# Performance work log

Measured on AMD Instinct MI355X. Metric: run time of the kernel, lower is better.

Reference implementation:

```python
import jax, jax.numpy as jnp
import numpy as np

N_HEADS = 16
NEG_BIG = float(-2**32 + 1)  # value the original writes into masked positions


def setup_inputs() -> dict:
    key = jax.random.key(0)
    ks = jax.random.split(key, 5)
    B, T, D = 64, 256, 1024
    s = 1.0 / np.sqrt(D)
    return {
        "x": jax.random.normal(ks[0], (B, T, D), jnp.float32),
        "pos_emb": jax.random.normal(ks[1], (T, D), jnp.float32),
        "Wq": jax.random.normal(ks[2], (D, D), jnp.float32) * s,
        "Wk": jax.random.normal(ks[3], (D, D), jnp.float32) * s,
        "Wv": jax.random.normal(ks[4], (D, D), jnp.float32) * s,
    }


def reference(x, pos_emb, Wq, Wk, Wv):
    B, T, D = x.shape
    H = N_HEADS
    dh = D // H
    # add position embeddings (same arange positions for every batch row)
    temporal = x + pos_emb[None, :T, :]            # [B, T, D]
    q = temporal @ Wq                              # [B, T, D]
    k = temporal @ Wk
    v = temporal @ Wv
    # chunk along feature dim into H heads, concatenate along batch dim -> [H*B, T, dh]
    def split_heads(t):
        return jnp.concatenate(jnp.split(t, H, axis=2), axis=0)
    q_, k_, v_ = split_heads(q), split_heads(k), split_heads(v)
    scores = jnp.einsum('btd,bsd->bts', q_, k_) / jnp.sqrt(jnp.asarray(T, x.dtype))  # [H*B, T, T]
    # original masks the LOWER triangle (tril > 0 -> padding), faithful to source
    tril = jnp.tril(jnp.ones((T, T), x.dtype))
    scores = jnp.where(tril > 0, jnp.asarray(NEG_BIG, x.dtype), scores)
    # original applies softmax over dim=0 (the batch*head axis), faithful to source
    probs = jax.nn.softmax(scores, axis=0)         # [H*B, T, T]
    out = jnp.einsum('bts,bsd->btd', probs, v_)    # [H*B, T, dh]
    # merge heads back: chunk along batch dim, concatenate along feature dim
    out = jnp.concatenate(jnp.split(out, H, axis=0), axis=-1)  # [B, T, D]
    return out
```

## Files before the change

kernel.cpp:

```cpp
#include <hip/hip_runtime.h>

constexpr int SEQ = 256;
constexpr int DIM = 1024;
constexpr float SCALE = 0.0625f;

typedef __attribute__((ext_vector_type(8))) short bf16x8;
typedef __attribute__((ext_vector_type(4))) float f32x4;
typedef unsigned short ushort_t;
typedef unsigned int uint_t;

__device__ __forceinline__ void gld_lds16(const void* g, void* l) {
  __builtin_amdgcn_global_load_lds(
      (const __attribute__((address_space(1))) unsigned int*)g,
      (__attribute__((address_space(3))) unsigned int*)l, 16, 0, 0);
}

__device__ __forceinline__ ushort_t f2bf(float f) {
  uint_t u = __float_as_uint(f);
  return (ushort_t)((u + 0x7fffu + ((u >> 16) & 1u)) >> 16);
}

__global__ __launch_bounds__(256)
void prep_a(const float* __restrict__ x, const float* __restrict__ pos,
            ushort_t* __restrict__ Ab) {
  const size_t idx = ((size_t)blockIdx.x * 256 + threadIdx.x) * 8;
  const int m = (int)(idx >> 10), k = (int)(idx & 1023);
  float4 x0 = *(const float4*)(x + idx);
  float4 x1 = *(const float4*)(x + idx + 4);
  const float* pp = pos + ((size_t)(m & 255) << 10) + k;
  float4 p0 = *(const float4*)pp;
  float4 p1 = *(const float4*)(pp + 4);
  uint_t w0 = (uint_t)f2bf(x0.x + p0.x) | ((uint_t)f2bf(x0.y + p0.y) << 16);
  uint_t w1 = (uint_t)f2bf(x0.z + p0.z) | ((uint_t)f2bf(x0.w + p0.w) << 16);
  uint_t w2 = (uint_t)f2bf(x1.x + p1.x) | ((uint_t)f2bf(x1.y + p1.y) << 16);
  uint_t w3 = (uint_t)f2bf(x1.z + p1.z) | ((uint_t)f2bf(x1.w + p1.w) << 16);
  *(uint4*)&Ab[idx] = make_uint4(w0, w1, w2, w3);
}

__global__ __launch_bounds__(256)
void pack_w(const float* __restrict__ Wq, const float* __restrict__ Wk,
            const float* __restrict__ Wv, ushort_t* __restrict__ Bp) {
  const float* W = (blockIdx.z == 0) ? Wq : (blockIdx.z == 1) ? Wk : Wv;
  const int n  = blockIdx.x * 256 + threadIdx.x;
  const int k8 = blockIdx.y * 8;
  uint_t h[8];
#pragma unroll
  for (int i = 0; i < 8; ++i) h[i] = f2bf(W[(size_t)(k8 + i) * DIM + n]);
  uint_t hp[4];
#pragma unroll
  for (int j = 0; j < 4; ++j) hp[j] = h[2 * j] | (h[2 * j + 1] << 16);
  const int np = blockIdx.z * 1024 + n;
  const int nb = np >> 8, nl = np & 255;
  const int kc = k8 >> 6, kk = k8 & 63;
  size_t base = (((size_t)nb * 16 + kc) * 256 + nl) * 64 + kk;
  *(uint4*)&Bp[base] = make_uint4(hp[0], hp[1], hp[2], hp[3]);
}

__global__ __launch_bounds__(512, 2)
void qkv_mfma(const ushort_t* __restrict__ Ab, const ushort_t* __restrict__ Bp,
              ushort_t* __restrict__ q_bf, ushort_t* __restrict__ k_bf,
              ushort_t* __restrict__ vT_bf) {
  const int id = (int)blockIdx.x;
  const int q8 = id >> 3;
  const int nb = q8 % 12;
  const int mb = (id & 7) * 8 + q8 / 12;
  const int tid = (int)threadIdx.x;
  const int wave = tid >> 6, lane = tid & 63;
  const int wm = wave >> 2, wn = wave & 3;
  const int l15 = lane & 15, quad = lane >> 4;

  __shared__ ushort_t smem[65536];

  const int r8 = lane >> 3;
  const int lc8 = ((lane & 7) ^ r8) * 8;
  const size_t a_row = ((size_t)(mb * 256 + wave * 8 + r8)) << 10;
  const size_t b_row = ((size_t)((nb * 16) * 256 + wave * 8 + r8)) << 6;
  const int wb = wave * 512;

#define SA(q, tt, c) gld_lds16(Ab + a_row + ((size_t)(q) << 16) + (size_t)(tt) * 64 + lc8, \
                               smem + (c) * 32768 + (q) * 4096 + wb)
#define SB(q, tt, c) gld_lds16(Bp + b_row + (size_t)(tt) * 16384 + (q) * 4096 + lc8, \
                               smem + (c) * 32768 + 16384 + (q) * 4096 + wb)

  const int swz = l15 & 7;
  const int cko0 = (quad ^ swz) * 8;
  const int cko1 = ((4 + quad) ^ swz) * 8;
  const int arow0 = (wm * 128 + l15) * 64;
  const int brow0 = (wn * 64 + l15) * 64;

  f32x4 acc[8][4] = {};
  bf16x8 af[4][2], bf[4][2];

#define LDA_II(IH, ii) do { \
    const int ro = arow0 + ((IH) * 64 + (ii) * 16) * 64; \
    af[ii][0] = *(const bf16x8*)&Ac[ro + cko0]; \
    af[ii][1] = *(const bf16x8*)&Ac[ro + cko1]; } while (0)
#define LDB_J(J) do { const int ro = brow0 + (J) * 1024; \
    bf[J][0] = *(const bf16x8*)&Bc[ro + cko0]; \
    bf[J][1] = *(const bf16x8*)&Bc[ro + cko1]; } while (0)
#define MMQ(IH, II0, II1, J0) do { \
    _Pragma("unroll") for (int ks = 0; ks < 2; ++ks) \
    _Pragma("unroll") for (int ii = (II0); ii < (II1); ++ii) \
    _Pragma("unroll") for (int jj = 0; jj < 2; ++jj) \
      acc[(IH) * 4 + ii][(J0) + jj] = __builtin_amdgcn_mfma_f32_16x16x32_bf16( \
          af[ii][ks], bf[(J0) + jj][ks], acc[(IH) * 4 + ii][(J0) + jj], 0, 0, 0); \
    } while (0)

  SA(0, 0, 0); SA(2, 0, 0); SB(0, 0, 0); SB(1, 0, 0); SB(2, 0, 0); SB(3, 0, 0);
  SA(1, 0, 0); SA(3, 0, 0);
  SB(0, 1, 1); SB(1, 1, 1); SA(0, 1, 1); SA(2, 1, 1);
  asm volatile("s_waitcnt vmcnt(6)" ::: "memory");
  __builtin_amdgcn_s_barrier();

  for (int t = 0; t < 16; ++t) {
    const int cur = t & 1, nxt = cur ^ 1;
    const int tn  = (t < 15) ? t + 1 : 15;
    const int tn2 = (t < 14) ? t + 2 : 15;
    const ushort_t* Ac = &smem[cur * 32768];
    const ushort_t* Bc = Ac + 16384;
    LDA_II(0, 0); LDA_II(0, 1); LDA_II(0, 2); LDA_II(0, 3);
    LDB_J(0); LDB_J(1);
    SB(2, tn, nxt); SB(3, tn, nxt);
    __builtin_amdgcn_s_barrier();
    LDB_J(2); LDB_J(3);
    SA(1, tn, nxt); SA(3, tn, nxt);
    asm volatile("s_waitcnt lgkmcnt(4)" ::: "memory");
    __builtin_amdgcn_s_setprio(1);
    MMQ(0, 0, 4, 0);
    __builtin_amdgcn_s_setprio(0);
    asm volatile("s_waitcnt vmcnt(8)" ::: "memory");
    __builtin_amdgcn_s_barrier();
    asm volatile("s_waitcnt lgkmcnt(0)" ::: "memory");
    __builtin_amdgcn_s_setprio(1);
    MMQ(0, 0, 2, 2);
    __builtin_amdgcn_s_setprio(0);
    LDA_II(1, 0); LDA_II(1, 1);
    __builtin_amdgcn_s_setprio(1);
    MMQ(0, 2, 4, 2);
    __builtin_amdgcn_s_setprio(0);
    LDA_II(1, 2); LDA_II(1, 3);
    __builtin_amdgcn_s_barrier();
    SB(0, tn2, cur); SB(1, tn2, cur);
    asm volatile("s_waitcnt lgkmcnt(0)" ::: "memory");
    __builtin_amdgcn_s_setprio(1);
    MMQ(1, 0, 4, 2);
    __builtin_amdgcn_s_setprio(0);
    __builtin_amdgcn_s_barrier();
    SA(0, tn2, cur); SA(2, tn2, cur);
    __builtin_amdgcn_s_setprio(1);
    MMQ(1, 0, 4, 0);
    __builtin_amdgcn_s_setprio(0);
    asm volatile("s_waitcnt vmcnt(6)" ::: "memory");
    __builtin_amdgcn_s_barrier();
  }

  asm volatile("s_waitcnt vmcnt(0)" ::: "memory");
  const int wq = nb >> 2;
  const int h  = (nb & 3) * 4 + wn;
  if (wq < 2) {
    ushort_t* base = ((wq == 0) ? q_bf : k_bf) + (size_t)(mb * 16 + h) * (SEQ * 64);
    const int tb = wm * 128 + quad * 4;
#pragma unroll
    for (int i = 0; i < 8; ++i)
#pragma unroll
      for (int j = 0; j < 4; ++j) {
        const int d = j * 16 + l15;
#pragma unroll
        for (int r = 0; r < 4; ++r)
          base[(size_t)(tb + i * 16 + r) * 64 + d] = f2bf(acc[i][j][r]);
      }
  } else {
    __builtin_amdgcn_s_barrier();
    ushort_t* L = &smem[wave * 4608];
    ushort_t* vbase = vT_bf + (size_t)(mb * 16 + h) * (64 * SEQ) + wm * 128;
    const int tc = (lane & 7) * 8;
#pragma unroll
    for (int g = 0; g < 2; ++g) {
#pragma unroll
      for (int ii = 0; ii < 4; ++ii)
#pragma unroll
        for (int j = 0; j < 4; ++j) {
          f32x4 v = acc[g * 4 + ii][j];
          uint_t lo = (uint_t)f2bf(v[0]) | ((uint_t)f2bf(v[1]) << 16);
          uint_t hi = (uint_t)f2bf(v[2]) | ((uint_t)f2bf(v[3]) << 16);
          *(uint2*)&L[(j * 16 + l15) * 72 + ii * 16 + quad * 4] = make_uint2(lo, hi);
        }
#pragma unroll
      for (int u = 0; u < 8; ++u) {
        const int d = u * 8 + r8;
        uint4 val = *(const uint4*)&L[d * 72 + tc];
        *(uint4*)&vbase[(size_t)d * SEQ + g * 64 + tc] = val;
      }
    }
  }
#undef SA
#undef SB
#undef LDA_II
#undef LDB_J
#undef MMQ
}

__global__ __launch_bounds__(256)
void stats_mfma(const ushort_t* __restrict__ qb, const ushort_t* __restrict__ kb,
                float* __restrict__ part_l) {
  const int p = blockIdx.x, g = blockIdx.y;
  int tt, ss;
  if (p < 4) { tt = p; ss = p; }
  else {
    const int idx = p - 4;
    tt = (idx < 3) ? 0 : (idx < 5) ? 1 : 2;
    ss = (idx < 3) ? idx + 1 : (idx < 5) ? idx - 1 : 3;
  }
  const bool diag = (p < 4);
  const int tid = threadIdx.x, wave = tid >> 6, lane = tid & 63;
  const int l15 = lane & 15, quad = lane >> 4;

  __shared__ __attribute__((aligned(16))) float red[4][64 * 68];

  f32x4 lacc[4][4] = {};

  for (int i4 = 0; i4 < 8; ++i4) {
    const int bp = g * 32 + wave * 8 + i4;
    const int bh = (bp & 63) * 16 + (bp >> 6);
    const ushort_t* qt = qb + (size_t)bh * (SEQ * 64) + (size_t)(tt * 64) * 64;
    const ushort_t* kt = kb + (size_t)bh * (SEQ * 64) + (size_t)(ss * 64) * 64;
    bf16x8 aq[4][2], bk[4][2];
#pragma unroll
    for (int m = 0; m < 4; ++m)
#pragma unroll
      for (int ks = 0; ks < 2; ++ks) {
        aq[m][ks] = *(const bf16x8*)&qt[(m * 16 + l15) * 64 + ks * 32 + quad * 8];
        bk[m][ks] = *(const bf16x8*)&kt[(m * 16 + l15) * 64 + ks * 32 + quad * 8];
      }
    f32x4 sf[4][4] = {};
#pragma unroll
    for (int ks = 0; ks < 2; ++ks)
#pragma unroll
      for (int m = 0; m < 4; ++m)
#pragma unroll
        for (int n = 0; n < 4; ++n)
          sf[m][n] = __builtin_amdgcn_mfma_f32_16x16x32_bf16(aq[m][ks], bk[n][ks], sf[m][n], 0, 0, 0);
#pragma unroll
    for (int m = 0; m < 4; ++m)
#pragma unroll
      for (int n = 0; n < 4; ++n)
#pragma unroll
        for (int r = 0; r < 4; ++r) {
          float e = __expf(sf[m][n][r] * SCALE);
          if (diag) {
            const int t = tt * 64 + m * 16 + quad * 4 + r;
            const int s = ss * 64 + n * 16 + l15;
            e = (s > t) ? e : 1.0f;
          }
          lacc[m][n][r] += e;
        }
  }
  float* R = red[wave];
#pragma unroll
  for (int m = 0; m < 4; ++m)
#pragma unroll
    for (int r = 0; r < 4; ++r) {
      const int row = m * 16 + quad * 4 + r;
#pragma unroll
      for (int n = 0; n < 4; ++n)
        R[row * 68 + n * 16 + l15] = lacc[m][n][r];
    }
  __syncthreads();
  const int trow = tid >> 2, c0 = (tid & 3) * 16;
  const float* r0 = &red[0][trow * 68 + c0];
  const float* r1 = &red[1][trow * 68 + c0];
  const float* r2 = &red[2][trow * 68 + c0];
  const float* r3 = &red[3][trow * 68 + c0];
  float* pl = part_l + (size_t)g * (SEQ * SEQ) + (size_t)(tt * 64 + trow) * SEQ + ss * 64 + c0;
#pragma unroll
  for (int c = 0; c < 16; c += 4) {
    float4 s0 = *(const float4*)&r0[c];
    float4 s1 = *(const float4*)&r1[c];
    float4 s2 = *(const float4*)&r2[c];
    float4 s3 = *(const float4*)&r3[c];
    float4 o;
    o.x = (s0.x + s1.x) + (s2.x + s3.x);
    o.y = (s0.y + s1.y) + (s2.y + s3.y);
    o.z = (s0.z + s1.z) + (s2.z + s3.z);
    o.w = (s0.w + s1.w) + (s2.w + s3.w);
    *(float4*)&pl[c] = o;
  }
}

__global__ __launch_bounds__(256)
void merge_kernel(const float* __restrict__ part_l, float* __restrict__ inv_lT) {
  const int i = blockIdx.x * 256 + threadIdx.x;
  const int t = i >> 8, s = i & 255;
  float invv;
  if (s <= t) invv = 1.0f / 1024.0f;
  else {
    const float* p = part_l + i;
    float a0 = 0.f, a1 = 0.f, a2 = 0.f, a3 = 0.f,
          a4 = 0.f, a5 = 0.f, a6 = 0.f, a7 = 0.f;
    for (int g = 0; g < 32; g += 8) {
      const float* q = p + ((size_t)g << 16);
      a0 += q[0ull << 16]; a1 += q[1ull << 16]; a2 += q[2ull << 16]; a3 += q[3ull << 16];
      a4 += q[4ull << 16]; a5 += q[5ull << 16]; a6 += q[6ull << 16]; a7 += q[7ull << 16];
    }
    invv = 1.0f / (((a0 + a1) + (a2 + a3)) + ((a4 + a5) + (a6 + a7)));
  }
  inv_lT[s * SEQ + t] = invv;
}

__global__ __launch_bounds__(256)
void pv_mfma(const ushort_t* __restrict__ qb, const ushort_t* __restrict__ kb,
             const ushort_t* __restrict__ vtb, const float* __restrict__ inv_lT,
             float* __restrict__ out) {
  const int bh = blockIdx.x;
  const int b = bh >> 4, h = bh & 15;
  const int tid = threadIdx.x, wave = tid >> 6, lane = tid & 63;
  const int l15 = lane & 15, quad = lane >> 4;
  const int t0 = wave * 64;

  __shared__ ushort_t Plds[4][64][72];
  ushort_t (*Pw)[72] = Plds[wave];

  const ushort_t* qq = qb + (size_t)bh * (SEQ * 64);
  const ushort_t* kk = kb + (size_t)bh * (SEQ * 64);
  const ushort_t* vv = vtb + (size_t)bh * (64 * SEQ);

  bf16x8 qf[4][2];
#pragma unroll
  for (int nt = 0; nt < 4; ++nt)
#pragma unroll
    for (int ks = 0; ks < 2; ++ks)
      qf[nt][ks] = *(const bf16x8*)&qq[(t0 + nt * 16 + l15) * 64 + ks * 32 + quad * 8];

  f32x4 o[4][4] = {};

  for (int sc = 0; sc < 4; ++sc) {
    if (sc < wave) {
      const uint_t c = 0x3A803A80u;
      const uint4 cc = make_uint4(c, c, c, c);
#pragma unroll
      for (int u = 0; u < 8; ++u) *(uint4*)&Pw[lane][u * 8] = cc;
    } else {
      bf16x8 kf[4][2];
#pragma unroll
      for (int ms = 0; ms < 4; ++ms)
#pragma unroll
        for (int ks = 0; ks < 2; ++ks)
          kf[ms][ks] = *(const bf16x8*)&kk[(sc * 64 + ms * 16 + l15) * 64 + ks * 32 + quad * 8];
      f32x4 sf[4][4] = {};
#pragma unroll
      for (int ks = 0; ks < 2; ++ks)
#pragma unroll
        for (int ms = 0; ms < 4; ++ms)
#pragma unroll
          for (int nt = 0; nt < 4; ++nt)
            sf[ms][nt] = __builtin_amdgcn_mfma_f32_16x16x32_bf16(kf[ms][ks], qf[nt][ks], sf[ms][nt], 0, 0, 0);
      const bool dg = (sc == wave);
      const int t = t0 + l15;
#pragma unroll
      for (int ms = 0; ms < 4; ++ms)
#pragma unroll
        for (int nt = 0; nt < 4; ++nt) {
          const int sb = sc * 64 + ms * 16 + quad * 4;
          const int tc = t + nt * 16;
          ushort_t pb[4];
#pragma unroll
          for (int r = 0; r < 4; ++r) {
            const int s = sb + r;
            float e = __expf(sf[ms][nt][r] * SCALE);
            if (dg) e = (s > tc) ? e : 1.0f;
            pb[r] = f2bf(e * inv_lT[(size_t)s * SEQ + tc]);
          }
          uint_t lo = (uint_t)pb[0] | ((uint_t)pb[1] << 16);
          uint_t hi = (uint_t)pb[2] | ((uint_t)pb[3] << 16);
          *(uint2*)&Pw[nt * 16 + l15][ms * 16 + quad * 4] = make_uint2(lo, hi);
        }
    }
    bf16x8 vf[4][2], pf[4][2];
#pragma unroll
    for (int nd = 0; nd < 4; ++nd)
#pragma unroll
      for (int ks = 0; ks < 2; ++ks)
        vf[nd][ks] = *(const bf16x8*)&vv[(nd * 16 + l15) * SEQ + sc * 64 + ks * 32 + quad * 8];
#pragma unroll
    for (int mt = 0; mt < 4; ++mt)
#pragma unroll
      for (int ks = 0; ks < 2; ++ks)
        pf[mt][ks] = *(const bf16x8*)&Pw[mt * 16 + l15][ks * 32 + quad * 8];
#pragma unroll
    for (int ks = 0; ks < 2; ++ks)
#pragma unroll
      for (int mt = 0; mt < 4; ++mt)
#pragma unroll
        for (int nd = 0; nd < 4; ++nd)
          o[mt][nd] = __builtin_amdgcn_mfma_f32_16x16x32_bf16(pf[mt][ks], vf[nd][ks], o[mt][nd], 0, 0, 0);
  }

  float* ob = out + (size_t)b * SEQ * DIM + h * 64;
#pragma unroll
  for (int mt = 0; mt < 4; ++mt)
#pragma unroll
    for (int r = 0; r < 4; ++r) {
      const int t = t0 + mt * 16 + quad * 4 + r;
#pragma unroll
      for (int nd = 0; nd < 4; ++nd)
        ob[(size_t)t * DIM + nd * 16 + l15] = o[mt][nd][r];
    }
}

extern "C" void kernel_launch(void* const* d_in, const int* in_sizes, int n_in,
                              void* d_out, int out_size, void* d_ws, size_t ws_size,
                              hipStream_t stream) {
  const float* x   = (const float*)d_in[0];
  const float* pos = (const float*)d_in[1];
  const float* Wq  = (const float*)d_in[2];
  const float* Wk  = (const float*)d_in[3];
  const float* Wv  = (const float*)d_in[4];
  float* out = (float*)d_out;

  ushort_t* Ab = (ushort_t*)d_out;
  ushort_t* Bp = (ushort_t*)((char*)d_out + 33554432);

  char* W = (char*)d_ws;
  ushort_t* q_bf   = (ushort_t*)(W);
  ushort_t* k_bf   = (ushort_t*)(W + 33554432);
  ushort_t* vT_bf  = (ushort_t*)(W + 67108864);
  float*    part_l = (float*)  (W + 100663296);
  float*    inv_lT = (float*)  (W + 167772160);

  prep_a<<<dim3(8192), 256, 0, stream>>>(x, pos, Ab);
  pack_w<<<dim3(4, 128, 3), 256, 0, stream>>>(Wq, Wk, Wv, Bp);
  qkv_mfma<<<dim3(768), 512, 0, stream>>>(Ab, Bp, q_bf, k_bf, vT_bf);
  stats_mfma<<<dim3(10, 32), 256, 0, stream>>>(q_bf, k_bf, part_l);
  merge_kernel<<<dim3(SEQ * SEQ / 256), 256, 0, stream>>>(part_l, inv_lT);
  pv_mfma<<<dim3(1024), 256, 0, stream>>>(q_bf, k_bf, vT_bf, inv_lT, out);
}
```

Measured before the change: 339.8 us.

## Skip masked PV chunks via precomputed V column sums; merge prep kernels

In the PV kernel, each wave no longer builds constant-probability tiles for fully masked chunks or runs their MFMAs. It instead adds 1/1024 times the column sum of V over those rows, computed once per block into shared memory. This relies on masked entries having uniform probability 1/(H*B) across the softmax axis. Separately, the activation prep and weight packing kernels are merged into one launch, saving one launch. Costs are an extra V read per block and a block-wide barrier.

```diff
diff --git a/kernel.cpp b/kernel.cpp
--- a/kernel.cpp
+++ b/kernel.cpp
@@ -20,40 +20,49 @@
   return (ushort_t)((u + 0x7fffu + ((u >> 16) & 1u)) >> 16);
 }
 
+__device__ __forceinline__ float bf2f(ushort_t h) {
+  return __uint_as_float(((uint_t)h) << 16);
+}
+
 __global__ __launch_bounds__(256)
-void prep_a(const float* __restrict__ x, const float* __restrict__ pos,
-            ushort_t* __restrict__ Ab) {
-  const size_t idx = ((size_t)blockIdx.x * 256 + threadIdx.x) * 8;
-  const int m = (int)(idx >> 10), k = (int)(idx & 1023);
-  float4 x0 = *(const float4*)(x + idx);
-  float4 x1 = *(const float4*)(x + idx + 4);
-  const float* pp = pos + ((size_t)(m & 255) << 10) + k;
-  float4 p0 = *(const float4*)pp;
-  float4 p1 = *(const float4*)(pp + 4);
-  uint_t w0 = (uint_t)f2bf(x0.x + p0.x) | ((uint_t)f2bf(x0.y + p0.y) << 16);
-  uint_t w1 = (uint_t)f2bf(x0.z + p0.z) | ((uint_t)f2bf(x0.w + p0.w) << 16);
-  uint_t w2 = (uint_t)f2bf(x1.x + p1.x) | ((uint_t)f2bf(x1.y + p1.y) << 16);
-  uint_t w3 = (uint_t)f2bf(x1.z + p1.z) | ((uint_t)f2bf(x1.w + p1.w) << 16);
-  *(uint4*)&Ab[idx] = make_uint4(w0, w1, w2, w3);
-}
-
-__global__ __launch_bounds__(256)
-void pack_w(const float* __restrict__ Wq, const float* __restrict__ Wk,
-            const float* __restrict__ Wv, ushort_t* __restrict__ Bp) {
-  const float* W = (blockIdx.z == 0) ? Wq : (blockIdx.z == 1) ? Wk : Wv;
-  const int n  = blockIdx.x * 256 + threadIdx.x;
-  const int k8 = blockIdx.y * 8;
-  uint_t h[8];
-#pragma unroll
-  for (int i = 0; i < 8; ++i) h[i] = f2bf(W[(size_t)(k8 + i) * DIM + n]);
-  uint_t hp[4];
-#pragma unroll
-  for (int j = 0; j < 4; ++j) hp[j] = h[2 * j] | (h[2 * j + 1] << 16);
-  const int np = blockIdx.z * 1024 + n;
-  const int nb = np >> 8, nl = np & 255;
-  const int kc = k8 >> 6, kk = k8 & 63;
-  size_t base = (((size_t)nb * 16 + kc) * 256 + nl) * 64 + kk;
-  *(uint4*)&Bp[base] = make_uint4(hp[0], hp[1], hp[2], hp[3]);
+void prep_pack(const float* __restrict__ x, const float* __restrict__ pos,
+               const float* __restrict__ Wq, const float* __restrict__ Wk,
+               const float* __restrict__ Wv,
+               ushort_t* __restrict__ Ab, ushort_t* __restrict__ Bp) {
+  const int bid = (int)blockIdx.x;
+  if (bid < 8192) {
+    const size_t idx = ((size_t)bid * 256 + threadIdx.x) * 8;
+    const int m = (int)(idx >> 10), k = (int)(idx & 1023);
+    float4 x0 = *(const float4*)(x + idx);
+    float4 x1 = *(const float4*)(x + idx + 4);
+    const float* pp = pos + ((size_t)(m & 255) << 10) + k;
+    float4 p0 = *(const float4*)pp;
+    float4 p1 = *(const float4*)(pp + 4);
+    uint_t w0 = (uint_t)f2bf(x0.x + p0.x) | ((uint_t)f2bf(x0.y + p0.y) << 16);
+    uint_t w1 = (uint_t)f2bf(x0.z + p0.z) | ((uint_t)f2bf(x0.w + p0.w) << 16);
+    uint_t w2 = (uint_t)f2bf(x1.x + p1.x) | ((uint_t)f2bf(x1.y + p1.y) << 16);
+    uint_t w3 = (uint_t)f2bf(x1.z + p1.z) | ((uint_t)f2bf(x1.w + p1.w) << 16);
+    *(uint4*)&Ab[idx] = make_uint4(w0, w1, w2, w3);
+  } else {
+    const int pid = bid - 8192;
+    const int z = pid >> 9;
+    const int rem = pid & 511;
+    const int by = rem >> 2, bx = rem & 3;
+    const float* W = (z == 0) ? Wq : (z == 1) ? Wk : Wv;
+    const int n  = bx * 256 + threadIdx.x;
+    const int k8 = by * 8;
+    uint_t h[8];
+#pragma unroll
+    for (int i = 0; i < 8; ++i) h[i] = f2bf(W[(size_t)(k8 + i) * DIM + n]);
+    uint_t hp[4];
+#pragma unroll
+    for (int j = 0; j < 4; ++j) hp[j] = h[2 * j] | (h[2 * j + 1] << 16);
+    const int np = z * 1024 + n;
+    const int nb = np >> 8, nl = np & 255;
+    const int kc = k8 >> 6, kk = k8 & 63;
+    size_t base = (((size_t)nb * 16 + kc) * 256 + nl) * 64 + kk;
+    *(uint4*)&Bp[base] = make_uint4(hp[0], hp[1], hp[2], hp[3]);
+  }
 }
 
 __global__ __launch_bounds__(512, 2)
@@ -318,12 +327,26 @@
   const int t0 = wave * 64;
 
   __shared__ ushort_t Plds[4][64][72];
+  __shared__ float csumL[4][64];
   ushort_t (*Pw)[72] = Plds[wave];
 
   const ushort_t* qq = qb + (size_t)bh * (SEQ * 64);
   const ushort_t* kk = kb + (size_t)bh * (SEQ * 64);
   const ushort_t* vv = vtb + (size_t)bh * (64 * SEQ);
 
+  {
+    const int d = lane;
+    const ushort_t* vr = vv + (size_t)d * SEQ + wave * 64;
+    float s = 0.f;
+#pragma unroll
+    for (int j = 0; j < 8; ++j) {
+      bf16x8 v8 = *(const bf16x8*)&vr[j * 8];
+#pragma unroll
+      for (int e = 0; e < 8; ++e) s += bf2f((ushort_t)v8[e]);
+    }
+    csumL[wave][d] = s;
+  }
+
   bf16x8 qf[4][2];
 #pragma unroll
   for (int nt = 0; nt < 4; ++nt)
@@ -331,50 +354,46 @@
     for (int ks = 0; ks < 2; ++ks)
       qf[nt][ks] = *(const bf16x8*)&qq[(t0 + nt * 16 + l15) * 64 + ks * 32 + quad * 8];
 
+  __syncthreads();
+
   f32x4 o[4][4] = {};
 
-  for (int sc = 0; sc < 4; ++sc) {
-    if (sc < wave) {
-      const uint_t c = 0x3A803A80u;
-      const uint4 cc = make_uint4(c, c, c, c);
-#pragma unroll
-      for (int u = 0; u < 8; ++u) *(uint4*)&Pw[lane][u * 8] = cc;
-    } else {
-      bf16x8 kf[4][2];
+  for (int sc = wave; sc < 4; ++sc) {
+    bf16x8 kf[4][2];
+#pragma unroll
+    for (int ms = 0; ms < 4; ++ms)
+#pragma unroll
+      for (int ks = 0; ks < 2; ++ks)
+        kf[ms][ks] = *(const bf16x8*)&kk[(sc * 64 + ms * 16 + l15) * 64 + ks * 32 + quad * 8];
+    f32x4 sf[4][4] = {};
+#pragma unroll
+    for (int ks = 0; ks < 2; ++ks)
 #pragma unroll
       for (int ms = 0; ms < 4; ++ms)
 #pragma unroll
-        for (int ks = 0; ks < 2; ++ks)
-          kf[ms][ks] = *(const bf16x8*)&kk[(sc * 64 + ms * 16 + l15) * 64 + ks * 32 + quad * 8];
-      f32x4 sf[4][4] = {};
-#pragma unroll
-      for (int ks = 0; ks < 2; ++ks)
-#pragma unroll
-        for (int ms = 0; ms < 4; ++ms)
-#pragma unroll
-          for (int nt = 0; nt < 4; ++nt)
-            sf[ms][nt] = __builtin_amdgcn_mfma_f32_16x16x32_bf16(kf[ms][ks], qf[nt][ks], sf[ms][nt], 0, 0, 0);
-      const bool dg = (sc == wave);
-      const int t = t0 + l15;
-#pragma unroll
-      for (int ms = 0; ms < 4; ++ms)
-#pragma unroll
-        for (int nt = 0; nt < 4; ++nt) {
-          const int sb = sc * 64 + ms * 16 + quad * 4;
-          const int tc = t + nt * 16;
-          ushort_t pb[4];
-#pragma unroll
-          for (int r = 0; r < 4; ++r) {
-            const int s = sb + r;
-            float e = __expf(sf[ms][nt][r] * SCALE);
-            if (dg) e = (s > tc) ? e : 1.0f;
-            pb[r] = f2bf(e * inv_lT[(size_t)s * SEQ + tc]);
-          }
-          uint_t lo = (uint_t)pb[0] | ((uint_t)pb[1] << 16);
-          uint_t hi = (uint_t)pb[2] | ((uint_t)pb[3] << 16);
-          *(uint2*)&Pw[nt * 16 + l15][ms * 16 + quad * 4] = make_uint2(lo, hi);
+        for (int nt = 0; nt < 4; ++nt)
+          sf[ms][nt] = __builtin_amdgcn_mfma_f32_16x16x32_bf16(kf[ms][ks], qf[nt][ks], sf[ms][nt], 0, 0, 0);
+    const bool dg = (sc == wave);
+    const int t = t0 + l15;
+#pragma unroll
+    for (int ms = 0; ms < 4; ++ms)
+#pragma unroll
+      for (int nt = 0; nt < 4; ++nt) {
+        const int sb = sc * 64 + ms * 16 + quad * 4;
+        const int tc = t + nt * 16;
+        ushort_t pb[4];
+#pragma unroll
+        for (int r = 0; r < 4; ++r) {
+          const int s = sb + r;
+          float e = __expf(sf[ms][nt][r] * SCALE);
+          if (dg) e = (s > tc) ? e : 1.0f;
+          pb[r] = f2bf(e * inv_lT[(size_t)s * SEQ + tc]);
         }
-    }
+        uint_t lo = (uint_t)pb[0] | ((uint_t)pb[1] << 16);
+        uint_t hi = (uint_t)pb[2] | ((uint_t)pb[3] << 16);
+        *(uint2*)&Pw[nt * 16 + l15][ms * 16 + quad * 4] = make_uint2(lo, hi);
+      }
+
     bf16x8 vf[4][2], pf[4][2];
 #pragma unroll
     for (int nd = 0; nd < 4; ++nd)
@@ -393,6 +412,19 @@
 #pragma unroll
         for (int nd = 0; nd < 4; ++nd)
           o[mt][nd] = __builtin_amdgcn_mfma_f32_16x16x32_bf16(pf[mt][ks], vf[nd][ks], o[mt][nd], 0, 0, 0);
+  }
+
+#pragma unroll
+  for (int nd = 0; nd < 4; ++nd) {
+    const int d = nd * 16 + l15;
+    float pref = 0.f;
+    for (int w2 = 0; w2 < wave; ++w2) pref += csumL[w2][d];
+    const float cc = pref * (1.0f / 1024.0f);
+#pragma unroll
+    for (int mt = 0; mt < 4; ++mt)
+#pragma unroll
+      for (int r = 0; r < 4; ++r)
+        o[mt][nd][r] += cc;
   }
 
   float* ob = out + (size_t)b * SEQ * DIM + h * 64;
@@ -427,8 +459,7 @@
   float*    part_l = (float*)  (W + 100663296);
   float*    inv_lT = (float*)  (W + 167772160);
 
-  prep_a<<<dim3(8192), 256, 0, stream>>>(x, pos, Ab);
-  pack_w<<<dim3(4, 128, 3), 256, 0, stream>>>(Wq, Wk, Wv, Bp);
+  prep_pack<<<dim3(9728), 256, 0, stream>>>(x, pos, Wq, Wk, Wv, Ab, Bp);
   qkv_mfma<<<dim3(768), 512, 0, stream>>>(Ab, Bp, q_bf, k_bf, vT_bf);
   stats_mfma<<<dim3(10, 32), 256, 0, stream>>>(q_bf, k_bf, part_l);
   merge_kernel<<<dim3(SEQ * SEQ / 256), 256, 0, stream>>>(part_l, inv_lT);
```

Result: faster. 323.8 us (-4.7%).
